# Kernel optimization log

Hardware: AMD Instinct MI355X
Metric: run time of the kernel (lower is better)

The kernel has to match this reference:

```python
import jax, jax.numpy as jnp
import numpy as np

B, S, DIN, DOUT = 4, 4096, 2048, 8192


def setup_inputs() -> dict:
    key = jax.random.key(0)
    k1, k2 = jax.random.split(key)
    x = jax.random.normal(k1, (B, S, DIN), dtype=jnp.float32)
    # kaiming_normal_ (fan_in mode, leaky_relu a=sqrt(5) default -> gain based) approx via std = sqrt(2/fan_in)
    weight = jax.random.normal(k2, (DOUT, DIN), dtype=jnp.float32) * np.sqrt(2.0 / DIN)
    bias = jnp.zeros((DOUT,), dtype=jnp.float32)
    gamma = jnp.ones((DIN,), dtype=jnp.float32)
    return {"x": x, "weight": weight, "bias": bias, "gamma": gamma}


def reference(x, weight, bias, gamma):
    # RMSNorm in fp32 (torch nn.RMSNorm, eps=None -> finfo(fp32).eps)
    eps = jnp.asarray(np.finfo(np.float32).eps, dtype=jnp.float32)
    ms = jnp.mean(x * x, axis=-1, keepdims=True)  # [B,S,1]
    xn = x * jax.lax.rsqrt(ms + eps) * gamma      # [B,S,DIN]
    # Ternary quantize weights: threshold = mean(|w|), values in {-1,0,+1}; STE for grads
    thr = jnp.mean(jnp.abs(weight))
    w_t = jnp.sign(weight) * (jnp.abs(weight) > thr).astype(weight.dtype)
    w = weight + jax.lax.stop_gradient(w_t - weight)
    # Linear: out = xn @ w.T + bias
    out = jnp.einsum('bsi,oi->bso', xn, w) + bias
    return out
```

## Files before the change

kernel.cpp:

```cpp
#include <hip/hip_runtime.h>

typedef unsigned short u16;
typedef unsigned int   u32;
typedef unsigned char  u8;
typedef __attribute__((ext_vector_type(4))) int   i32x4;

constexpr int B_ = 4, S_ = 4096, DIN_ = 2048, DOUT_ = 8192;
constexpr int M_ = B_ * S_;
constexpr int N_ = DOUT_;
constexpr int K_ = DIN_;
constexpr size_t NW_ = (size_t)DOUT_ * DIN_;

#define GPTR(p) ((const __attribute__((address_space(1))) void*)(p))
#define LPTR(p) ((__attribute__((address_space(3))) void*)(p))

#define SB0()   __builtin_amdgcn_sched_barrier(0)
#define BAR()   asm volatile("s_barrier" ::: "memory")
#define LGKM0() asm volatile("s_waitcnt lgkmcnt(0)" ::: "memory")
#define VM4()   asm volatile("s_waitcnt vmcnt(4)" ::: "memory")
#define VM0()   asm volatile("s_waitcnt vmcnt(0)" ::: "memory")

__global__ __launch_bounds__(256)
void abssum_kernel(const float* __restrict__ w, double* __restrict__ partials)
{
    const int tid = threadIdx.x;
    const float* base = w + (size_t)blockIdx.x * 16384 + tid * 4;
    double s = 0.0;
#pragma unroll
    for (int i = 0; i < 16; ++i) {
        float4 v = *(const float4*)(base + i * 1024);
        s += (double)fabsf(v.x) + (double)fabsf(v.y)
           + (double)fabsf(v.z) + (double)fabsf(v.w);
    }
#pragma unroll
    for (int o = 32; o; o >>= 1) s += __shfl_xor(s, o, 64);
    __shared__ double red[4];
    if ((tid & 63) == 0) red[tid >> 6] = s;
    __syncthreads();
    if (tid == 0) partials[blockIdx.x] = (red[0] + red[1]) + (red[2] + red[3]);
}

__global__ __launch_bounds__(1024)
void finalize_thr(const double* __restrict__ partials, double* __restrict__ thr)
{
    __shared__ double red[1024];
    const int tid = threadIdx.x;
    red[tid] = partials[tid];
    __syncthreads();
    for (int s = 512; s > 0; s >>= 1) {
        if (tid < s) red[tid] += red[tid + s];
        __syncthreads();
    }
    if (tid == 0) *thr = red[0] * (1.0 / (double)NW_);
}

__global__ __launch_bounds__(256)
void prep_kernel(const float* __restrict__ x, const float* __restrict__ gamma,
                 const double* __restrict__ thr_p, const float* __restrict__ w,
                 signed char* __restrict__ wt,
                 signed char* __restrict__ xn, float* __restrict__ scale)
{
    __shared__ float redsum[4];
    __shared__ float redmax[4];
    const int tid = threadIdx.x;

    if (blockIdx.x >= (unsigned)M_) {
        const double thr = *thr_p;
        const size_t i = ((size_t)(blockIdx.x - M_) * 256 + tid) * 4;
        float4 v = *(const float4*)(w + i);
        union { signed char c[4]; u32 u; } p;
        p.c[0] = (signed char)((fabs((double)v.x) > thr) ? (v.x > 0.0f ? 1 : -1) : 0);
        p.c[1] = (signed char)((fabs((double)v.y) > thr) ? (v.y > 0.0f ? 1 : -1) : 0);
        p.c[2] = (signed char)((fabs((double)v.z) > thr) ? (v.z > 0.0f ? 1 : -1) : 0);
        p.c[3] = (signed char)((fabs((double)v.w) > thr) ? (v.w > 0.0f ? 1 : -1) : 0);
        *(u32*)(wt + i) = p.u;
        return;
    }

    const int row = blockIdx.x;
    const float* xr = x + (size_t)row * K_;
    float4 a = *(const float4*)(xr + tid * 8);
    float4 b = *(const float4*)(xr + tid * 8 + 4);
    float s = a.x*a.x + a.y*a.y + a.z*a.z + a.w*a.w
            + b.x*b.x + b.y*b.y + b.z*b.z + b.w*b.w;
#pragma unroll
    for (int o = 32; o; o >>= 1) s += __shfl_xor(s, o, 64);
    if ((tid & 63) == 0) redsum[tid >> 6] = s;
    __syncthreads();
    const float tot = (redsum[0] + redsum[1]) + (redsum[2] + redsum[3]);
    const float r = rsqrtf(tot * (1.0f / (float)K_) + 1.1920928955078125e-07f);
    float4 g0 = *(const float4*)(gamma + tid * 8);
    float4 g1 = *(const float4*)(gamma + tid * 8 + 4);
    float v[8];
    v[0] = a.x * r * g0.x;  v[1] = a.y * r * g0.y;
    v[2] = a.z * r * g0.z;  v[3] = a.w * r * g0.w;
    v[4] = b.x * r * g1.x;  v[5] = b.y * r * g1.y;
    v[6] = b.z * r * g1.z;  v[7] = b.w * r * g1.w;
    float m = 0.0f;
#pragma unroll
    for (int j = 0; j < 8; ++j) m = fmaxf(m, fabsf(v[j]));
#pragma unroll
    for (int o = 32; o; o >>= 1) m = fmaxf(m, __shfl_xor(m, o, 64));
    if ((tid & 63) == 0) redmax[tid >> 6] = m;
    __syncthreads();
    const float rowmax = fmaxf(fmaxf(redmax[0], redmax[1]), fmaxf(redmax[2], redmax[3]));
    const float inv = rowmax > 0.0f ? 127.0f / rowmax : 0.0f;
    union { signed char c[8]; uint2 u; } p;
#pragma unroll
    for (int j = 0; j < 8; ++j) p.c[j] = (signed char)__float2int_rn(v[j] * inv);
    *(uint2*)(xn + (size_t)row * K_ + tid * 8) = p.u;
    if (tid == 0) scale[row] = rowmax * (1.0f / 127.0f);
}

__global__ __launch_bounds__(256, 2)
void gemm_bt_kernel(const u8* __restrict__ A, const u8* __restrict__ Bt,
                    const float* __restrict__ bias, const float* __restrict__ scale,
                    float* __restrict__ C)
{
    __shared__ alignas(16) u8 sm[65536];
    const char* smc = (const char*)sm;

    const int tid  = threadIdx.x;
    const int lane = tid & 63;
    const int wid  = tid >> 6;
    const int wm   = wid >> 1;
    const int wn   = wid & 1;
    const int hi   = lane >> 4;

    const int swz = (blockIdx.x & 7) * 1024 + (blockIdx.x >> 3);
    const int gm0 = (swz >> 6) * 128;
    const int gn0 = (swz & 63) * 128;

    const int cswel = ((tid & 7) ^ ((tid >> 3) & 7)) * 16;
    const u8* gA = A  + (size_t)(gm0 + (tid >> 3)) * K_ + cswel;
    const u8* gB = Bt + (size_t)(gn0 + (tid >> 3)) * K_ + cswel;

    auto STAGE2 = [&](const u8* g, int ldsb, int kt, int j) {
        u8* d = sm + ldsb + j * 4096 + tid * 16;
        const u8* s = g + (size_t)j * 32 * K_ + kt;
        __builtin_amdgcn_global_load_lds(GPTR(s),                   LPTR(d),        16, 0, 0);
        __builtin_amdgcn_global_load_lds(GPTR(s + (size_t)32 * K_), LPTR(d + 4096), 16, 0, 0);
    };
#define ABUF(b) ((b) * 16384)
#define BBUF(b) (32768 + (b) * 16384)

    const int c0 = ((hi ^ (lane & 7)) << 4);
    const int rowbyteA = (wm * 64 + (lane & 15)) * 128;
    const int rowbyteB = (wn * 64 + (lane & 15)) * 128;

#define RA(bufr, m, kk) (*(const i32x4*)(smc + (bufr)*16384 + rowbyteA + (m)*2048 + (c0 ^ ((kk) << 6))))
#define RB(bufr, n, kk) (*(const i32x4*)(smc + 32768 + (bufr)*16384 + rowbyteB + (n)*2048 + (c0 ^ ((kk) << 6))))

    i32x4 acc[4][4] = {};
    i32x4 a0[2][2], a1[2][2], b0[2][2], b1[2][2];

#define MFMA_BLK(AF, BF, MO, NO)                                                   \
    do {                                                                           \
        _Pragma("unroll") for (int kk = 0; kk < 2; ++kk)                           \
        _Pragma("unroll") for (int m = 0; m < 2; ++m)                              \
        _Pragma("unroll") for (int n = 0; n < 2; ++n)                              \
            acc[m + MO][n + NO] = __builtin_amdgcn_mfma_i32_16x16x64_i8(           \
                AF[m][kk], BF[n][kk], acc[m + MO][n + NO], 0, 0, 0);               \
    } while (0)

#define READ_A0B0(bufr)                                                            \
    do {                                                                           \
        _Pragma("unroll") for (int m = 0; m < 2; ++m) {                            \
            a0[m][0] = RA(bufr, m, 0); a0[m][1] = RA(bufr, m, 1); }                \
        _Pragma("unroll") for (int n = 0; n < 2; ++n) {                            \
            b0[n][0] = RB(bufr, n, 0); b0[n][1] = RB(bufr, n, 1); }                \
    } while (0)
#define READ_A1(bufr)                                                              \
    do { _Pragma("unroll") for (int m = 0; m < 2; ++m) {                           \
            a1[m][0] = RA(bufr, m + 2, 0); a1[m][1] = RA(bufr, m + 2, 1); } } while (0)
#define READ_B1(bufr)                                                              \
    do { _Pragma("unroll") for (int n = 0; n < 2; ++n) {                           \
            b1[n][0] = RB(bufr, n + 2, 0); b1[n][1] = RB(bufr, n + 2, 1); } } while (0)

#define PRIO_MFMA(AF, BF, MO, NO)                                                  \
    do { __builtin_amdgcn_s_setprio(1); MFMA_BLK(AF, BF, MO, NO);                  \
         __builtin_amdgcn_s_setprio(0); } while (0)

    STAGE2(gA, ABUF(0), 0, 0);   STAGE2(gA, ABUF(0), 0, 2);
    STAGE2(gB, BBUF(0), 0, 0);   STAGE2(gB, BBUF(0), 0, 2);
    STAGE2(gA, ABUF(1), 128, 0); STAGE2(gA, ABUF(1), 128, 2);
    VM4(); SB0(); BAR();

    for (int i = 0; i < 8; ++i) {
        const int kt1  = i * 256 + 128;
        const int ktn0 = i * 256 + 256;
        const int ktn1 = i * 256 + 384;
        const bool f = (i < 7);

        READ_A0B0(0);
        STAGE2(gB, BBUF(1), kt1, 0);
        SB0(); BAR(); LGKM0(); SB0();
        PRIO_MFMA(a0, b0, 0, 0);
        SB0(); BAR();

        READ_A1(0);
        STAGE2(gB, BBUF(1), kt1, 2);
        SB0(); BAR(); LGKM0(); SB0();
        PRIO_MFMA(a1, b0, 2, 0);
        SB0(); BAR();

        READ_B1(0);
        if (f) STAGE2(gA, ABUF(0), ktn0, 0);
        SB0(); BAR(); LGKM0(); SB0();
        PRIO_MFMA(a0, b1, 0, 2);
        SB0(); BAR();

        if (f) STAGE2(gA, ABUF(0), ktn0, 2);
        SB0(); BAR();
        PRIO_MFMA(a1, b1, 2, 2);
        SB0();
        if (f) { VM4(); } else { VM0(); }
        SB0(); BAR();

        READ_A0B0(1);
        if (f) STAGE2(gB, BBUF(0), ktn0, 0);
        SB0(); BAR(); LGKM0(); SB0();
        PRIO_MFMA(a0, b0, 0, 0);
        SB0(); BAR();

        READ_A1(1);
        if (f) STAGE2(gB, BBUF(0), ktn0, 2);
        SB0(); BAR(); LGKM0(); SB0();
        PRIO_MFMA(a1, b0, 2, 0);
        SB0(); BAR();

        READ_B1(1);
        if (f) STAGE2(gA, ABUF(1), ktn1, 0);
        SB0(); BAR(); LGKM0(); SB0();
        PRIO_MFMA(a0, b1, 0, 2);
        SB0(); BAR();

        if (f) STAGE2(gA, ABUF(1), ktn1, 2);
        SB0(); BAR();
        PRIO_MFMA(a1, b1, 2, 2);
        SB0();
        if (f) { VM4(); }
        SB0(); BAR();
    }

    const int orow0 = gm0 + wm * 64 + hi * 4;
    const int ocol0 = gn0 + wn * 64 + (lane & 15);
    float bv[4];
#pragma unroll
    for (int n = 0; n < 4; ++n) bv[n] = bias[ocol0 + n * 16];
#pragma unroll
    for (int m = 0; m < 4; ++m) {
#pragma unroll
        for (int ri = 0; ri < 4; ++ri) {
            const int row = orow0 + m * 16 + ri;
            const float sc = scale[row];
#pragma unroll
            for (int n = 0; n < 4; ++n) {
                C[(size_t)row * N_ + (ocol0 + n * 16)] = (float)acc[m][n][ri] * sc + bv[n];
            }
        }
    }
#undef RA
#undef RB
#undef MFMA_BLK
#undef READ_A0B0
#undef READ_A1
#undef READ_B1
#undef PRIO_MFMA
#undef ABUF
#undef BBUF
}

extern "C" void kernel_launch(void* const* d_in, const int* in_sizes, int n_in,
                              void* d_out, int out_size, void* d_ws, size_t ws_size,
                              hipStream_t stream)
{
    const float* x     = (const float*)d_in[0];
    const float* w     = (const float*)d_in[1];
    const float* bias  = (const float*)d_in[2];
    const float* gamma = (const float*)d_in[3];
    float* out = (float*)d_out;

    char* ws = (char*)d_ws;
    double*      thr      = (double*)(ws);
    double*      partials = (double*)(ws + 1024);
    signed char* wt       = (signed char*)(ws + 16384);
    signed char* xn       = (signed char*)(ws + 16384 + NW_);
    float*       scale    = (float*)(ws + 16384 + NW_ + (size_t)M_ * K_);

    abssum_kernel <<<1024,  256,  0, stream>>>(w, partials);
    finalize_thr  <<<1,     1024, 0, stream>>>(partials, thr);
    prep_kernel   <<<M_ + 16384, 256, 0, stream>>>(x, gamma, thr, w, wt, xn, scale);
    gemm_bt_kernel<<<(M_/128)*(N_/128), 256, 0, stream>>>((const u8*)xn, (const u8*)wt, bias, scale, out);
}
```

Measured before the change: 484.1 us.

## Retile int8 GEMM to 256x128 blocks with 512 threads and K-step 64

The int8 MFMA GEMM moves from 128x128 tiles with 256 threads and a 128-byte K step to 256x128 tiles with 8 waves and a 64-byte K step. The LDS layout, swizzle, staging and vmcnt accounting are rewritten to match, and LDS use drops to 48KB per block. The goal is more reuse of each B tile, more waves in flight to hide latency, and fewer blocks overall. The trade-off is twice as many barrier-separated phases per K, and launch bounds of (512,4) that may squeeze registers and force spills. The fused prep kernel is also split into separate ternarize and RMSNorm-quantize launches.

```diff
diff --git a/kernel.cpp b/kernel.cpp
--- a/kernel.cpp
+++ b/kernel.cpp
@@ -17,7 +17,7 @@
 #define SB0()   __builtin_amdgcn_sched_barrier(0)
 #define BAR()   asm volatile("s_barrier" ::: "memory")
 #define LGKM0() asm volatile("s_waitcnt lgkmcnt(0)" ::: "memory")
-#define VM4()   asm volatile("s_waitcnt vmcnt(4)" ::: "memory")
+#define VM2()   asm volatile("s_waitcnt vmcnt(2)" ::: "memory")
 #define VM0()   asm volatile("s_waitcnt vmcnt(0)" ::: "memory")
 
 __global__ __launch_bounds__(256)
@@ -55,29 +55,26 @@
 }
 
 __global__ __launch_bounds__(256)
-void prep_kernel(const float* __restrict__ x, const float* __restrict__ gamma,
-                 const double* __restrict__ thr_p, const float* __restrict__ w,
-                 signed char* __restrict__ wt,
-                 signed char* __restrict__ xn, float* __restrict__ scale)
-{
-    __shared__ float redsum[4];
-    __shared__ float redmax[4];
+void ternarize_kernel(const float* __restrict__ w, const double* __restrict__ thr_p,
+                      signed char* __restrict__ wt)
+{
+    const double thr = *thr_p;
+    const size_t i = ((size_t)blockIdx.x * 256 + threadIdx.x) * 4;
+    float4 v = *(const float4*)(w + i);
+    union { signed char c[4]; u32 u; } p;
+    p.c[0] = (signed char)((fabs((double)v.x) > thr) ? (v.x > 0.0f ? 1 : -1) : 0);
+    p.c[1] = (signed char)((fabs((double)v.y) > thr) ? (v.y > 0.0f ? 1 : -1) : 0);
+    p.c[2] = (signed char)((fabs((double)v.z) > thr) ? (v.z > 0.0f ? 1 : -1) : 0);
+    p.c[3] = (signed char)((fabs((double)v.w) > thr) ? (v.w > 0.0f ? 1 : -1) : 0);
+    *(u32*)(wt + i) = p.u;
+}
+
+__global__ __launch_bounds__(256)
+void rmsnorm_q_kernel(const float* __restrict__ x, const float* __restrict__ gamma,
+                      signed char* __restrict__ xn, float* __restrict__ scale)
+{
+    const int row = blockIdx.x;
     const int tid = threadIdx.x;
-
-    if (blockIdx.x >= (unsigned)M_) {
-        const double thr = *thr_p;
-        const size_t i = ((size_t)(blockIdx.x - M_) * 256 + tid) * 4;
-        float4 v = *(const float4*)(w + i);
-        union { signed char c[4]; u32 u; } p;
-        p.c[0] = (signed char)((fabs((double)v.x) > thr) ? (v.x > 0.0f ? 1 : -1) : 0);
-        p.c[1] = (signed char)((fabs((double)v.y) > thr) ? (v.y > 0.0f ? 1 : -1) : 0);
-        p.c[2] = (signed char)((fabs((double)v.z) > thr) ? (v.z > 0.0f ? 1 : -1) : 0);
-        p.c[3] = (signed char)((fabs((double)v.w) > thr) ? (v.w > 0.0f ? 1 : -1) : 0);
-        *(u32*)(wt + i) = p.u;
-        return;
-    }
-
-    const int row = blockIdx.x;
     const float* xr = x + (size_t)row * K_;
     float4 a = *(const float4*)(xr + tid * 8);
     float4 b = *(const float4*)(xr + tid * 8 + 4);
@@ -85,6 +82,8 @@
             + b.x*b.x + b.y*b.y + b.z*b.z + b.w*b.w;
 #pragma unroll
     for (int o = 32; o; o >>= 1) s += __shfl_xor(s, o, 64);
+    __shared__ float redsum[4];
+    __shared__ float redmax[4];
     if ((tid & 63) == 0) redsum[tid >> 6] = s;
     __syncthreads();
     const float tot = (redsum[0] + redsum[1]) + (redsum[2] + redsum[3]);
@@ -112,12 +111,12 @@
     if (tid == 0) scale[row] = rowmax * (1.0f / 127.0f);
 }
 
-__global__ __launch_bounds__(256, 2)
+__global__ __launch_bounds__(512, 4)
 void gemm_bt_kernel(const u8* __restrict__ A, const u8* __restrict__ Bt,
                     const float* __restrict__ bias, const float* __restrict__ scale,
                     float* __restrict__ C)
 {
-    __shared__ alignas(16) u8 sm[65536];
+    __shared__ alignas(16) u8 sm[49152];
     const char* smc = (const char*)sm;
 
     const int tid  = threadIdx.x;
@@ -127,119 +126,91 @@
     const int wn   = wid & 1;
     const int hi   = lane >> 4;
 
-    const int swz = (blockIdx.x & 7) * 1024 + (blockIdx.x >> 3);
-    const int gm0 = (swz >> 6) * 128;
+    const int swz = (blockIdx.x & 7) * 512 + (blockIdx.x >> 3);
+    const int gm0 = (swz >> 6) * 256;
     const int gn0 = (swz & 63) * 128;
 
-    const int cswel = ((tid & 7) ^ ((tid >> 3) & 7)) * 16;
-    const u8* gA = A  + (size_t)(gm0 + (tid >> 3)) * K_ + cswel;
-    const u8* gB = Bt + (size_t)(gn0 + (tid >> 3)) * K_ + cswel;
-
-    auto STAGE2 = [&](const u8* g, int ldsb, int kt, int j) {
-        u8* d = sm + ldsb + j * 4096 + tid * 16;
-        const u8* s = g + (size_t)j * 32 * K_ + kt;
-        __builtin_amdgcn_global_load_lds(GPTR(s),                   LPTR(d),        16, 0, 0);
-        __builtin_amdgcn_global_load_lds(GPTR(s + (size_t)32 * K_), LPTR(d + 4096), 16, 0, 0);
+    const int cswel = ((tid & 3) ^ ((tid >> 2) & 3)) * 16;
+    const int rbase = tid >> 2;
+    const u8* gA = A  + (size_t)(gm0 + rbase) * K_ + cswel;
+    const u8* gB = Bt + (size_t)(gn0 + rbase) * K_ + cswel;
+
+    auto STAGE_A = [&](int buf, int kb) {
+        u8* d = sm + buf * 16384 + tid * 16;
+        const u8* s = gA + kb;
+        __builtin_amdgcn_global_load_lds(GPTR(s),                    LPTR(d),        16, 0, 0);
+        __builtin_amdgcn_global_load_lds(GPTR(s + (size_t)128 * K_), LPTR(d + 8192), 16, 0, 0);
     };
-#define ABUF(b) ((b) * 16384)
-#define BBUF(b) (32768 + (b) * 16384)
-
-    const int c0 = ((hi ^ (lane & 7)) << 4);
-    const int rowbyteA = (wm * 64 + (lane & 15)) * 128;
-    const int rowbyteB = (wn * 64 + (lane & 15)) * 128;
-
-#define RA(bufr, m, kk) (*(const i32x4*)(smc + (bufr)*16384 + rowbyteA + (m)*2048 + (c0 ^ ((kk) << 6))))
-#define RB(bufr, n, kk) (*(const i32x4*)(smc + 32768 + (bufr)*16384 + rowbyteB + (n)*2048 + (c0 ^ ((kk) << 6))))
+    auto STAGE_B = [&](int buf, int kb) {
+        u8* d = sm + 32768 + buf * 8192 + tid * 16;
+        __builtin_amdgcn_global_load_lds(GPTR(gB + kb), LPTR(d), 16, 0, 0);
+    };
+
+    const int c0 = ((hi ^ (lane & 3)) << 4);
+    const int rowbyteA = (wm * 64 + (lane & 15)) * 64;
+    const int rowbyteB = (wn * 64 + (lane & 15)) * 64;
+
+#define RA(bufr, m) (*(const i32x4*)(smc + (bufr)*16384 + rowbyteA + (m)*1024 + c0))
+#define RB(bufr, n) (*(const i32x4*)(smc + 32768 + (bufr)*8192 + rowbyteB + (n)*1024 + c0))
 
     i32x4 acc[4][4] = {};
-    i32x4 a0[2][2], a1[2][2], b0[2][2], b1[2][2];
-
-#define MFMA_BLK(AF, BF, MO, NO)                                                   \
+    i32x4 a[4], b01[2], b23[2];
+
+#define MFMA_BLK(BF, NO)                                                           \
     do {                                                                           \
-        _Pragma("unroll") for (int kk = 0; kk < 2; ++kk)                           \
-        _Pragma("unroll") for (int m = 0; m < 2; ++m)                              \
+        _Pragma("unroll") for (int m = 0; m < 4; ++m)                              \
         _Pragma("unroll") for (int n = 0; n < 2; ++n)                              \
-            acc[m + MO][n + NO] = __builtin_amdgcn_mfma_i32_16x16x64_i8(           \
-                AF[m][kk], BF[n][kk], acc[m + MO][n + NO], 0, 0, 0);               \
+            acc[m][n + NO] = __builtin_amdgcn_mfma_i32_16x16x64_i8(                \
+                a[m], BF[n], acc[m][n + NO], 0, 0, 0);                             \
     } while (0)
 
-#define READ_A0B0(bufr)                                                            \
+#define READ_AB01(bufr)                                                            \
     do {                                                                           \
-        _Pragma("unroll") for (int m = 0; m < 2; ++m) {                            \
-            a0[m][0] = RA(bufr, m, 0); a0[m][1] = RA(bufr, m, 1); }                \
-        _Pragma("unroll") for (int n = 0; n < 2; ++n) {                            \
-            b0[n][0] = RB(bufr, n, 0); b0[n][1] = RB(bufr, n, 1); }                \
+        _Pragma("unroll") for (int m = 0; m < 4; ++m) a[m] = RA(bufr, m);          \
+        _Pragma("unroll") for (int n = 0; n < 2; ++n) b01[n] = RB(bufr, n);        \
     } while (0)
-#define READ_A1(bufr)                                                              \
-    do { _Pragma("unroll") for (int m = 0; m < 2; ++m) {                           \
-            a1[m][0] = RA(bufr, m + 2, 0); a1[m][1] = RA(bufr, m + 2, 1); } } while (0)
-#define READ_B1(bufr)                                                              \
-    do { _Pragma("unroll") for (int n = 0; n < 2; ++n) {                           \
-            b1[n][0] = RB(bufr, n + 2, 0); b1[n][1] = RB(bufr, n + 2, 1); } } while (0)
-
-#define PRIO_MFMA(AF, BF, MO, NO)                                                  \
-    do { __builtin_amdgcn_s_setprio(1); MFMA_BLK(AF, BF, MO, NO);                  \
+#define READ_B23(bufr)                                                             \
+    do { _Pragma("unroll") for (int n = 0; n < 2; ++n) b23[n] = RB(bufr, n + 2); } while (0)
+
+#define PRIO_MFMA(BF, NO)                                                          \
+    do { __builtin_amdgcn_s_setprio(1); MFMA_BLK(BF, NO);                          \
          __builtin_amdgcn_s_setprio(0); } while (0)
 
-    STAGE2(gA, ABUF(0), 0, 0);   STAGE2(gA, ABUF(0), 0, 2);
-    STAGE2(gB, BBUF(0), 0, 0);   STAGE2(gB, BBUF(0), 0, 2);
-    STAGE2(gA, ABUF(1), 128, 0); STAGE2(gA, ABUF(1), 128, 2);
-    VM4(); SB0(); BAR();
-
-    for (int i = 0; i < 8; ++i) {
-        const int kt1  = i * 256 + 128;
-        const int ktn0 = i * 256 + 256;
-        const int ktn1 = i * 256 + 384;
-        const bool f = (i < 7);
-
-        READ_A0B0(0);
-        STAGE2(gB, BBUF(1), kt1, 0);
-        SB0(); BAR(); LGKM0(); SB0();
-        PRIO_MFMA(a0, b0, 0, 0);
-        SB0(); BAR();
-
-        READ_A1(0);
-        STAGE2(gB, BBUF(1), kt1, 2);
-        SB0(); BAR(); LGKM0(); SB0();
-        PRIO_MFMA(a1, b0, 2, 0);
-        SB0(); BAR();
-
-        READ_B1(0);
-        if (f) STAGE2(gA, ABUF(0), ktn0, 0);
-        SB0(); BAR(); LGKM0(); SB0();
-        PRIO_MFMA(a0, b1, 0, 2);
-        SB0(); BAR();
-
-        if (f) STAGE2(gA, ABUF(0), ktn0, 2);
-        SB0(); BAR();
-        PRIO_MFMA(a1, b1, 2, 2);
+    STAGE_A(0, 0);
+    STAGE_B(0, 0);
+    STAGE_A(1, 64);
+    VM2(); SB0(); BAR();
+
+    for (int i = 0; i < 16; ++i) {
+        const int kb   = i * 128;
+        const bool f = (i < 15);
+
+        READ_AB01(0);
+        STAGE_B(1, kb + 64);
+        SB0(); BAR(); LGKM0(); SB0();
+        PRIO_MFMA(b01, 0);
+        SB0(); BAR();
+
+        READ_B23(0);
+        if (f) STAGE_A(0, kb + 128);
+        SB0(); BAR(); LGKM0(); SB0();
+        PRIO_MFMA(b23, 2);
         SB0();
-        if (f) { VM4(); } else { VM0(); }
-        SB0(); BAR();
-
-        READ_A0B0(1);
-        if (f) STAGE2(gB, BBUF(0), ktn0, 0);
-        SB0(); BAR(); LGKM0(); SB0();
-        PRIO_MFMA(a0, b0, 0, 0);
-        SB0(); BAR();
-
-        READ_A1(1);
-        if (f) STAGE2(gB, BBUF(0), ktn0, 2);
-        SB0(); BAR(); LGKM0(); SB0();
-        PRIO_MFMA(a1, b0, 2, 0);
-        SB0(); BAR();
-
-        READ_B1(1);
-        if (f) STAGE2(gA, ABUF(1), ktn1, 0);
-        SB0(); BAR(); LGKM0(); SB0();
-        PRIO_MFMA(a0, b1, 0, 2);
-        SB0(); BAR();
-
-        if (f) STAGE2(gA, ABUF(1), ktn1, 2);
-        SB0(); BAR();
-        PRIO_MFMA(a1, b1, 2, 2);
+        if (f) { VM2(); } else { VM0(); }
+        SB0(); BAR();
+
+        READ_AB01(1);
+        if (f) STAGE_B(0, kb + 128);
+        SB0(); BAR(); LGKM0(); SB0();
+        PRIO_MFMA(b01, 0);
+        SB0(); BAR();
+
+        READ_B23(1);
+        if (f) STAGE_A(1, kb + 192);
+        SB0(); BAR(); LGKM0(); SB0();
+        PRIO_MFMA(b23, 2);
         SB0();
-        if (f) { VM4(); }
+        if (f) { VM2(); }
         SB0(); BAR();
     }
 
@@ -263,12 +234,9 @@
 #undef RA
 #undef RB
 #undef MFMA_BLK
-#undef READ_A0B0
-#undef READ_A1
-#undef READ_B1
+#undef READ_AB01
+#undef READ_B23
 #undef PRIO_MFMA
-#undef ABUF
-#undef BBUF
 }
 
 extern "C" void kernel_launch(void* const* d_in, const int* in_sizes, int n_in,
@@ -288,8 +256,9 @@
     signed char* xn       = (signed char*)(ws + 16384 + NW_);
     float*       scale    = (float*)(ws + 16384 + NW_ + (size_t)M_ * K_);
 
-    abssum_kernel <<<1024,  256,  0, stream>>>(w, partials);
-    finalize_thr  <<<1,     1024, 0, stream>>>(partials, thr);
-    prep_kernel   <<<M_ + 16384, 256, 0, stream>>>(x, gamma, thr, w, wt, xn, scale);
-    gemm_bt_kernel<<<(M_/128)*(N_/128), 256, 0, stream>>>((const u8*)xn, (const u8*)wt, bias, scale, out);
-}
+    abssum_kernel   <<<1024,  256,  0, stream>>>(w, partials);
+    finalize_thr    <<<1,     1024, 0, stream>>>(partials, thr);
+    ternarize_kernel<<<16384, 256,  0, stream>>>(w, thr, wt);
+    rmsnorm_q_kernel<<<M_,    256,  0, stream>>>(x, gamma, xn, scale);
+    gemm_bt_kernel  <<<(M_/256)*(N_/128), 512, 0, stream>>>((const u8*)xn, (const u8*)wt, bias, scale, out);
+}
```

New measurement: 420.5 us. 13.1% less time.
